# Kernel tuning notes

Hardware: AMD Instinct MI355X
Metric: run time of the kernel (lower is better)

## Reference

```python
import jax, jax.numpy as jnp
import numpy as np

N, F_IN, E = 20000, 256, 320000
H, C = 8, 128            # conv1 heads, per-head channels
OUT, DH = 1, 128         # output_dim, dense_hidden
G = 64                   # number of graphs
EPS = 1e-5


def setup_inputs() -> dict:
    key = jax.random.key(0)
    ks = jax.random.split(key, 20)
    s = 0.05
    return {
        'x': jax.random.normal(ks[0], (N, F_IN), jnp.float32),
        'edge_index': jax.random.randint(ks[1], (2, E), 0, N, jnp.int64),
        'batch': jnp.sort(jax.random.randint(ks[2], (N,), 0, G, jnp.int64)),
        # conv1 (GATv2, heads=8, concat)
        'w1_l': jax.random.normal(ks[3], (F_IN, H * C), jnp.float32) * s,
        'w1_r': jax.random.normal(ks[4], (F_IN, H * C), jnp.float32) * s,
        'att1': jax.random.normal(ks[5], (H, C), jnp.float32) * s,
        'b1': jnp.zeros((H * C,), jnp.float32),
        # norm1 (BatchNorm over H*C features)
        'g1': jnp.ones((H * C,), jnp.float32),
        'be1': jnp.zeros((H * C,), jnp.float32),
        # conv2 (GATv2, heads=1, concat=False)
        'w2_l': jax.random.normal(ks[6], (H * C, OUT), jnp.float32) * s,
        'w2_r': jax.random.normal(ks[7], (H * C, OUT), jnp.float32) * s,
        'att2': jax.random.normal(ks[8], (1, OUT), jnp.float32) * s,
        'b2': jnp.zeros((OUT,), jnp.float32),
        # norm2
        'g2': jnp.ones((OUT,), jnp.float32),
        'be2': jnp.zeros((OUT,), jnp.float32),
        # MLP head
        'lw1': jax.random.normal(ks[9], (OUT, DH), jnp.float32) * s,
        'lb1': jnp.zeros((DH,), jnp.float32),
        'lw2': jax.random.normal(ks[10], (DH, OUT), jnp.float32) * s,
        'lb2': jnp.zeros((OUT,), jnp.float32),
    }


def gatv2(x, src, dst, wl, wr, att, bias, heads, ch, concat):
    n = x.shape[0]
    xl = (x @ wl).reshape(n, heads, ch)
    xr = (x @ wr).reshape(n, heads, ch)
    # edge-wise GATv2 score: a^T LeakyReLU(x_l[j] + x_r[i]), slope 0.2
    e = jnp.einsum('ehc,hc->eh', jax.nn.leaky_relu(xl[src] + xr[dst], 0.2), att)
    # segment softmax over incoming edges per target node
    emax = jax.ops.segment_max(e, dst, num_segments=n)
    ee = jnp.exp(e - emax[dst])
    denom = jax.ops.segment_sum(ee, dst, num_segments=n)
    alpha = ee / (denom[dst] + 1e-16)
    out = jax.ops.segment_sum(alpha[..., None] * xl[src], dst, num_segments=n)  # [n,h,c]
    if concat:
        return out.reshape(n, heads * ch) + bias
    return out.mean(axis=1) + bias


def batchnorm(x, g, b):
    mu = x.mean(axis=0)
    var = ((x - mu) ** 2).mean(axis=0)
    return (x - mu) * jax.lax.rsqrt(var + EPS) * g + b


def reference(x, edge_index, batch, w1_l, w1_r, att1, b1, g1, be1,
              w2_l, w2_r, att2, b2, g2, be2, lw1, lb1, lw2, lb2):
    n = x.shape[0]
    loops = jnp.arange(n, dtype=edge_index.dtype)
    src = jnp.concatenate([edge_index[0], loops])  # add self-loops (PyG default)
    dst = jnp.concatenate([edge_index[1], loops])

    h = gatv2(x, src, dst, w1_l, w1_r, att1, b1, H, C, concat=True)
    h = jax.nn.leaky_relu(batchnorm(h, g1, be1), 0.01)
    # dropout: eval mode (identity)
    h = gatv2(h, src, dst, w2_l, w2_r, att2, b2, 1, OUT, concat=False)
    h = jax.nn.leaky_relu(batchnorm(h, g2, be2), 0.01)

    # global mean pool over graphs
    sums = jax.ops.segment_sum(h, batch, num_segments=G)
    cnt = jax.ops.segment_sum(jnp.ones((n, 1), h.dtype), batch, num_segments=G)
    pooled = sums / jnp.maximum(cnt, 1.0)

    out = jax.nn.leaky_relu(pooled @ lw1 + lb1, 0.01)
    return out @ lw2 + lb2
```

## Files before the change

kernel.cpp:

```cpp
#include <hip/hip_runtime.h>
#include <hip/hip_bf16.h>


__device__ __forceinline__ float lrelu(float x, float s) { return x > 0.f ? x : s * x; }

typedef _Float16 half8 __attribute__((ext_vector_type(8)));
typedef _Float16 half4v __attribute__((ext_vector_type(4)));
typedef _Float16 half2v __attribute__((ext_vector_type(2)));
typedef float f32x4 __attribute__((ext_vector_type(4)));

#define GLOBAL_AS __attribute__((address_space(1)))
#define LDS_AS __attribute__((address_space(3)))

__device__ __forceinline__ void async_copy16(const void* g, void* l) {
  __builtin_amdgcn_global_load_lds((const GLOBAL_AS unsigned int*)g,
                                   (LDS_AS unsigned int*)l, 16, 0, 0);
}

__global__ void zero_ints(int* __restrict__ p, int n) {
  const int t = blockIdx.x * blockDim.x + threadIdx.x;
  if (t < n) p[t] = 0;
}

__global__ void edge_hist(const int* __restrict__ ei, int E, int N,
                          int* __restrict__ counts) {
  const int t = blockIdx.x * blockDim.x + threadIdx.x;
  if (t >= E + N) return;
  const int dst = (t < E) ? ei[E + t] : (t - E);
  atomicAdd(&counts[dst], 1);
}

__global__ __launch_bounds__(1024) void scan_counts(const int* __restrict__ counts,
                                                    int* __restrict__ row_ptr,
                                                    int* __restrict__ cursor, int N) {
  __shared__ int sdata[1024];
  __shared__ int lcnt[20480];
  const int t = threadIdx.x;
  if (N <= 20480) {
    for (int j = t; j < N; j += 1024) lcnt[j] = counts[j];
    __syncthreads();
    const int chunk = (N + 1023) / 1024;
    const int s0 = min(N, t * chunk);
    const int s1 = min(N, s0 + chunk);
    int lsum = 0;
    for (int i = s0; i < s1; ++i) lsum += lcnt[i];
    sdata[t] = lsum;
    __syncthreads();
    for (int off = 1; off < 1024; off <<= 1) {
      int v = 0;
      if (t >= off) v = sdata[t - off];
      __syncthreads();
      sdata[t] += v;
      __syncthreads();
    }
    int run = sdata[t] - lsum;
    for (int i = s0; i < s1; ++i) { const int c = lcnt[i]; lcnt[i] = run; run += c; }
    if (s0 < N && s1 == N) row_ptr[N] = run;
    __syncthreads();
    for (int j = t; j < N; j += 1024) {
      const int v = lcnt[j];
      row_ptr[j] = v;
      cursor[j] = v;
    }
  } else {
    const int chunk = (N + 1023) / 1024;
    const int s0 = min(N, t * chunk);
    const int s1 = min(N, s0 + chunk);
    int lsum = 0;
    for (int i = s0; i < s1; ++i) lsum += counts[i];
    sdata[t] = lsum;
    __syncthreads();
    for (int off = 1; off < 1024; off <<= 1) {
      int v = 0;
      if (t >= off) v = sdata[t - off];
      __syncthreads();
      sdata[t] += v;
      __syncthreads();
    }
    int run = sdata[t] - lsum;
    for (int i = s0; i < s1; ++i) {
      row_ptr[i] = run;
      cursor[i] = run;
      run += counts[i];
    }
    if (s0 < N && s1 == N) row_ptr[N] = run;
  }
}

__global__ void edge_scatter(const int* __restrict__ ei, int E, int N,
                             int* __restrict__ cursor, int* __restrict__ col) {
  const int t = blockIdx.x * blockDim.x + threadIdx.x;
  if (t >= E + N) return;
  const int dst = (t < E) ? ei[E + t] : (t - E);
  const int src = (t < E) ? ei[t] : (t - E);
  const int pos = atomicAdd(&cursor[dst], 1);
  col[pos] = src;
}

__global__ void convert_x(const float* __restrict__ x, _Float16* __restrict__ A2, int M) {
  const int t = blockIdx.x * blockDim.x + threadIdx.x;
  if (t >= M * 64) return;
  const int m = t >> 6;
  const int k4 = (t & 63) * 4;
  const float4 v = *(const float4*)(x + (size_t)m * 256 + k4);
  const float sx = 16.f;
  *(half4v*)(A2 + (size_t)m * 256 + k4) =
      (half4v){(_Float16)(v.x * sx), (_Float16)(v.y * sx),
               (_Float16)(v.z * sx), (_Float16)(v.w * sx)};
}

__global__ __launch_bounds__(256) void convert_w(const float* __restrict__ wl,
                                                 const float* __restrict__ wr,
                                                 _Float16* __restrict__ B2,
                                                 int colOff, int W) {
  const int n = blockIdx.x;
  const int k = threadIdx.x;
  const float v = 16.f * ((n < W) ? wl[k * 1024 + colOff + n]
                                  : wr[k * 1024 + colOff + (n - W)]);
  B2[(size_t)n * 256 + k] = (_Float16)v;
}

__global__ __launch_bounds__(256) void gemm_mfma(const _Float16* __restrict__ A2,
                                                 const _Float16* __restrict__ B2,
                                                 _Float16* __restrict__ C,
                                                 int M, int Ntot) {
  __shared__ __align__(16) _Float16 LDSbuf[2 * 128 * 64];
  _Float16* As = LDSbuf;
  _Float16* Bs = LDSbuf + 128 * 64;
  const int tid = threadIdx.x;
  const int lane = tid & 63;
  const int wv = tid >> 6;
  const int wm = wv & 1, wn = wv >> 1;
  const int m_blk = blockIdx.y * 128;
  const int n_blk = blockIdx.x * 128;
  const int row16 = lane & 15, quad = lane >> 4;
  f32x4 acc[4][4] = {};

  for (int kt = 0; kt < 4; ++kt) {
    const int kg = kt * 64;
#pragma unroll
    for (int j = 0; j < 4; ++j) {
      const int ci = j * 256 + tid;
      const int row = ci >> 3;
      const int c = ci & 7;
      const int gc = c ^ (row & 7);
      _Float16* ldsA = &As[(j * 256 + wv * 64) * 8];
      _Float16* ldsB = &Bs[(j * 256 + wv * 64) * 8];
      const int growA = min(m_blk + row, M - 1);
      async_copy16(A2 + (size_t)growA * 256 + kg + gc * 8, ldsA);
      async_copy16(B2 + (size_t)(n_blk + row) * 256 + kg + gc * 8, ldsB);
    }
    __syncthreads();
#pragma unroll
    for (int ks = 0; ks < 2; ++ks) {
      half8 af[4], bf[4];
#pragma unroll
      for (int mi = 0; mi < 4; ++mi) {
        const int r = wm * 64 + mi * 16 + row16;
        const int cl = (ks * 4 + quad) ^ (r & 7);
        af[mi] = *(const half8*)&As[r * 64 + cl * 8];
      }
#pragma unroll
      for (int ni = 0; ni < 4; ++ni) {
        const int r = wn * 64 + ni * 16 + row16;
        const int cl = (ks * 4 + quad) ^ (r & 7);
        bf[ni] = *(const half8*)&Bs[r * 64 + cl * 8];
      }
#pragma unroll
      for (int mi = 0; mi < 4; ++mi)
#pragma unroll
        for (int ni = 0; ni < 4; ++ni)
          acc[mi][ni] = __builtin_amdgcn_mfma_f32_16x16x32_f16(af[mi], bf[ni], acc[mi][ni], 0, 0, 0);
    }
    __syncthreads();
  }
  const float inv = 1.f / 256.f;
  _Float16* tw = LDSbuf + wv * 4096;
#pragma unroll
  for (int mi = 0; mi < 4; ++mi)
#pragma unroll
    for (int reg = 0; reg < 4; ++reg) {
      const int r_in = mi * 16 + quad * 4 + reg;
#pragma unroll
      for (int ni = 0; ni < 4; ++ni)
        tw[r_in * 64 + ni * 16 + row16] = (_Float16)(acc[mi][ni][reg] * inv);
    }
#pragma unroll
  for (int p8 = 0; p8 < 8; ++p8) {
    const int row = p8 * 8 + (lane >> 3);
    const int grow = m_blk + wm * 64 + row;
    if (grow < M) {
      const half8 v = *(const half8*)&tw[row * 64 + (lane & 7) * 8];
      *(half8*)(C + (size_t)grow * Ntot + n_blk + wn * 64 + (lane & 7) * 8) = v;
    }
  }
}

template <int CPT>
__global__ __launch_bounds__(256, 6) void conv1_attn(const _Float16* __restrict__ xlrp,
                                                     const int* __restrict__ row_ptr,
                                                     const int* __restrict__ col,
                                                     const float* __restrict__ att,
                                                     const float* __restrict__ bias,
                                                     _Float16* __restrict__ h1,
                                                     int W, int N) {
  constexpr int PAIRS = CPT / 2;
  constexpr int NV8 = CPT / 8;
  constexpr int HG = 128 / CPT;
  union H8 { half8 v; half2v p[4]; };
  const int lane = threadIdx.x & 63;
  const int i = blockIdx.x * 4 + (threadIdx.x >> 6);
  if (i >= N) return;
  const int f = lane * CPT;
  half2v a2[PAIRS], xr2[PAIRS];
  float acc[CPT];
#pragma unroll
  for (int p = 0; p < PAIRS; ++p)
    a2[p] = (half2v){(_Float16)att[f + 2 * p], (_Float16)att[f + 2 * p + 1]};
  {
    const half8* xrp = (const half8*)(xlrp + (size_t)i * (2 * W) + W + f);
#pragma unroll
    for (int j = 0; j < NV8; ++j) {
      H8 u; u.v = xrp[j];
#pragma unroll
      for (int k = 0; k < 4; ++k) xr2[j * 4 + k] = u.p[k];
    }
  }
#pragma unroll
  for (int c = 0; c < CPT; ++c) acc[c] = 0.f;
  float m = -3.0e38f, l = 0.f;
  const int kb = row_ptr[i];
  const int ke = row_ptr[i + 1];
  for (int base = kb; base < ke; base += 64) {
    const int cnt = min(64, ke - base);
    const int myc = (lane < cnt) ? col[base + lane] : 0;
    H8 xc[NV8], xn[NV8];
    {
      const int s0 = __shfl(myc, 0);
      const half8* rp = (const half8*)(xlrp + (size_t)s0 * (2 * W) + f);
#pragma unroll
      for (int j = 0; j < NV8; ++j) xc[j].v = rp[j];
    }
    for (int q = 0; q < cnt; ++q) {
      if (q + 1 < cnt) {
        const int sn = __shfl(myc, q + 1);
        const half8* rp = (const half8*)(xlrp + (size_t)sn * (2 * W) + f);
#pragma unroll
        for (int j = 0; j < NV8; ++j) xn[j].v = rp[j];
      }
      float s = 0.f;
#pragma unroll
      for (int p = 0; p < PAIRS; ++p) {
        const half2v xp = xc[p >> 2].p[p & 3];
        const half2v t = xp + xr2[p];
        const half2v t5 = t * (half2v){(_Float16)0.2f, (_Float16)0.2f};
        const half2v lr = __builtin_elementwise_max(t, t5);
        s = __builtin_amdgcn_fdot2(a2[p], lr, s, false);
      }
#pragma unroll
      for (int off = HG / 2; off >= 1; off >>= 1) s += __shfl_xor(s, off);
      if (s <= m) {
        const float pw = __expf(s - m);
        l += pw;
#pragma unroll
        for (int p = 0; p < PAIRS; ++p) {
          const half2v xp = xc[p >> 2].p[p & 3];
          acc[2 * p] += pw * (float)xp[0];
          acc[2 * p + 1] += pw * (float)xp[1];
        }
      } else {
        const float sc = __expf(m - s);
        m = s;
        l = l * sc + 1.f;
#pragma unroll
        for (int p = 0; p < PAIRS; ++p) {
          const half2v xp = xc[p >> 2].p[p & 3];
          acc[2 * p] = acc[2 * p] * sc + (float)xp[0];
          acc[2 * p + 1] = acc[2 * p + 1] * sc + (float)xp[1];
        }
      }
#pragma unroll
      for (int j = 0; j < NV8; ++j) xc[j] = xn[j];
    }
  }
  const float inv = 1.f / (l + 1e-16f);
  _Float16* outp = h1 + (size_t)i * 1024 + f;
#pragma unroll
  for (int j = 0; j < NV8; ++j) {
    H8 u;
#pragma unroll
    for (int k = 0; k < 4; ++k) {
      const int c = j * 8 + 2 * k;
      u.p[k] = (half2v){(_Float16)(acc[c] * inv + bias[f + c]),
                        (_Float16)(acc[c + 1] * inv + bias[f + c + 1])};
    }
    ((half8*)outp)[j] = u.v;
  }
}

__global__ __launch_bounds__(256) void bn1_stats(const _Float16* __restrict__ h1,
                                                 float* __restrict__ bsum,
                                                 float* __restrict__ bsq, int N) {
  const int f = threadIdx.x * 4;
  const int chunk = (N + 255) / 256;
  const int r0 = blockIdx.y * chunk;
  const int r1 = min(N, r0 + chunk);
  float s0 = 0.f, s1 = 0.f, s2 = 0.f, s3 = 0.f;
  float q0 = 0.f, q1 = 0.f, q2 = 0.f, q3 = 0.f;
  for (int r = r0; r < r1; ++r) {
    const half4v v4 = *(const half4v*)(h1 + (size_t)r * 1024 + f);
    const float v0 = (float)v4[0], v1 = (float)v4[1], v2 = (float)v4[2], v3 = (float)v4[3];
    s0 += v0; q0 += v0 * v0;
    s1 += v1; q1 += v1 * v1;
    s2 += v2; q2 += v2 * v2;
    s3 += v3; q3 += v3 * v3;
  }
  atomicAdd(&bsum[f + 0], s0); atomicAdd(&bsq[f + 0], q0);
  atomicAdd(&bsum[f + 1], s1); atomicAdd(&bsq[f + 1], q1);
  atomicAdd(&bsum[f + 2], s2); atomicAdd(&bsq[f + 2], q2);
  atomicAdd(&bsum[f + 3], s3); atomicAdd(&bsq[f + 3], q3);
}

__global__ __launch_bounds__(256) void bn1_proj(const _Float16* __restrict__ h1,
                                                const float* __restrict__ bsum,
                                                const float* __restrict__ bsq,
                                                const float* __restrict__ g1,
                                                const float* __restrict__ be1,
                                                const float* __restrict__ w2l,
                                                const float* __restrict__ w2r,
                                                float* __restrict__ xl2,
                                                float* __restrict__ xr2, int N) {
  const int i = blockIdx.x;
  const int tid = threadIdx.x;
  const int f = tid * 4;
  const half4v hv = *(const half4v*)(h1 + (size_t)i * 1024 + f);
  const float4 h4 = make_float4((float)hv[0], (float)hv[1], (float)hv[2], (float)hv[3]);
  const float4 s4 = *(const float4*)(bsum + f);
  const float4 q4 = *(const float4*)(bsq + f);
  const float4 g4 = *(const float4*)(g1 + f);
  const float4 b4 = *(const float4*)(be1 + f);
  const float4 wl = *(const float4*)(w2l + f);
  const float4 wr = *(const float4*)(w2r + f);
  const float invN = 1.f / (float)N;
  float pl = 0.f, pr = 0.f;
  {
    float mu, var, rs, v;
    mu = s4.x * invN; var = q4.x * invN - mu * mu; rs = 1.f / sqrtf(var + 1e-5f);
    v = lrelu((h4.x - mu) * rs * g4.x + b4.x, 0.01f); pl += v * wl.x; pr += v * wr.x;
    mu = s4.y * invN; var = q4.y * invN - mu * mu; rs = 1.f / sqrtf(var + 1e-5f);
    v = lrelu((h4.y - mu) * rs * g4.y + b4.y, 0.01f); pl += v * wl.y; pr += v * wr.y;
    mu = s4.z * invN; var = q4.z * invN - mu * mu; rs = 1.f / sqrtf(var + 1e-5f);
    v = lrelu((h4.z - mu) * rs * g4.z + b4.z, 0.01f); pl += v * wl.z; pr += v * wr.z;
    mu = s4.w * invN; var = q4.w * invN - mu * mu; rs = 1.f / sqrtf(var + 1e-5f);
    v = lrelu((h4.w - mu) * rs * g4.w + b4.w, 0.01f); pl += v * wl.w; pr += v * wr.w;
  }
#pragma unroll
  for (int off = 32; off; off >>= 1) {
    pl += __shfl_down(pl, off);
    pr += __shfl_down(pr, off);
  }
  __shared__ float sp[8];
  if ((tid & 63) == 0) {
    sp[tid >> 6] = pl;
    sp[4 + (tid >> 6)] = pr;
  }
  __syncthreads();
  if (tid == 0) {
    xl2[i] = sp[0] + sp[1] + sp[2] + sp[3];
    xr2[i] = sp[4] + sp[5] + sp[6] + sp[7];
  }
}

__global__ __launch_bounds__(256) void conv2_attn(const float* __restrict__ xl2,
                                                  const float* __restrict__ xr2,
                                                  const int* __restrict__ row_ptr,
                                                  const int* __restrict__ col,
                                                  const float* __restrict__ att2,
                                                  const float* __restrict__ b2,
                                                  float* __restrict__ out2,
                                                  float* __restrict__ bn2acc, int N) {
  const int i = blockIdx.x * blockDim.x + threadIdx.x;
  float val = 0.f;
  if (i < N) {
    const float a = att2[0];
    const float xr = xr2[i];
    float m = -3.0e38f, l = 0.f, acc = 0.f;
    const int kb = row_ptr[i];
    const int ke = row_ptr[i + 1];
    for (int k = kb; k < ke; ++k) {
      const float xv = xl2[col[k]];
      const float s = a * lrelu(xv + xr, 0.2f);
      const float mn = fmaxf(m, s);
      const float sc = __expf(m - mn);
      const float p = __expf(s - mn);
      l = l * sc + p;
      acc = acc * sc + p * xv;
      m = mn;
    }
    val = acc / (l + 1e-16f) + b2[0];
    out2[i] = val;
  }
  float s = (i < N) ? val : 0.f;
  float q = s * s;
#pragma unroll
  for (int off = 32; off; off >>= 1) {
    s += __shfl_down(s, off);
    q += __shfl_down(q, off);
  }
  __shared__ float red[8];
  if ((threadIdx.x & 63) == 0) {
    red[threadIdx.x >> 6] = s;
    red[4 + (threadIdx.x >> 6)] = q;
  }
  __syncthreads();
  if (threadIdx.x == 0) {
    atomicAdd(&bn2acc[0], red[0] + red[1] + red[2] + red[3]);
    atomicAdd(&bn2acc[1], red[4] + red[5] + red[6] + red[7]);
  }
}

__global__ __launch_bounds__(256) void bn2_pool(const float* __restrict__ out2,
                                                const float* __restrict__ bn2acc,
                                                const float* __restrict__ g2,
                                                const float* __restrict__ be2,
                                                const int* __restrict__ batch,
                                                float* __restrict__ pool_sum,
                                                float* __restrict__ pool_cnt, int N) {
  __shared__ float ls[64];
  __shared__ float lc[64];
  const int tid = threadIdx.x;
  if (tid < 64) { ls[tid] = 0.f; lc[tid] = 0.f; }
  __syncthreads();
  const int i = blockIdx.x * blockDim.x + tid;
  if (i < N) {
    const float invN = 1.f / (float)N;
    const float mu = bn2acc[0] * invN;
    const float var = bn2acc[1] * invN - mu * mu;
    const float rs = 1.f / sqrtf(var + 1e-5f);
    const float v = lrelu((out2[i] - mu) * rs * g2[0] + be2[0], 0.01f);
    const int g = batch[i];
    atomicAdd(&ls[g], v);
    atomicAdd(&lc[g], 1.f);
  }
  __syncthreads();
  if (tid < 64 && lc[tid] != 0.f) {
    atomicAdd(&pool_sum[tid], ls[tid]);
    atomicAdd(&pool_cnt[tid], lc[tid]);
  }
}

__global__ void head_mlp(const float* __restrict__ pool_sum, const float* __restrict__ pool_cnt,
                         const float* __restrict__ lw1, const float* __restrict__ lb1,
                         const float* __restrict__ lw2, const float* __restrict__ lb2,
                         float* __restrict__ out) {
  const int g = threadIdx.x;
  if (g >= 64) return;
  const float p = pool_sum[g] / fmaxf(pool_cnt[g], 1.f);
  float acc = 0.f;
  for (int d = 0; d < 128; ++d) {
    float t = p * lw1[d] + lb1[d];
    t = lrelu(t, 0.01f);
    acc += t * lw2[d];
  }
  out[g] = acc + lb2[0];
}

extern "C" void kernel_launch(void* const* d_in, const int* in_sizes, int n_in,
                              void* d_out, int out_size, void* d_ws, size_t ws_size,
                              hipStream_t stream) {
  const float* x = (const float*)d_in[0];
  const int* ei = (const int*)d_in[1];
  const int* batch = (const int*)d_in[2];
  const float* w1_l = (const float*)d_in[3];
  const float* w1_r = (const float*)d_in[4];
  const float* att1 = (const float*)d_in[5];
  const float* b1 = (const float*)d_in[6];
  const float* g1 = (const float*)d_in[7];
  const float* be1 = (const float*)d_in[8];
  const float* w2_l = (const float*)d_in[9];
  const float* w2_r = (const float*)d_in[10];
  const float* att2 = (const float*)d_in[11];
  const float* b2 = (const float*)d_in[12];
  const float* g2 = (const float*)d_in[13];
  const float* be2 = (const float*)d_in[14];
  const float* lw1 = (const float*)d_in[15];
  const float* lb1 = (const float*)d_in[16];
  const float* lw2 = (const float*)d_in[17];
  const float* lb2 = (const float*)d_in[18];

  const int N = in_sizes[2];
  const int E = in_sizes[1] / 2;
  const int ET = E + N;

  const size_t AL = 255;
  auto al = [&](size_t b) { return (b + AL) & ~AL; };
  const size_t zbytes = (size_t)N * 4 + 4096 + 4096 + 16 + 256 + 256;
  const size_t fixedNoXlr = al((size_t)N * 2048)
                          + 3 * al((size_t)N * 4)
                          + al((size_t)(N + 1) * 4)
                          + al((size_t)ET * 4)
                          + al((size_t)N * 4)
                          + al(zbytes);
  const size_t a2b = al((size_t)N * 256 * 2);
  int P = 1;
  while (P < 8) {
    const size_t xlrb = al((size_t)N * (4096 / P));
    const size_t b2b = al((size_t)(2 * (1024 / P)) * 256 * 2);
    const size_t extra = (P == 1) ? 0 : (a2b + b2b);
    if (fixedNoXlr + xlrb + extra <= ws_size) break;
    P <<= 1;
  }
  const int W = 1024 / P;

  char* ws = (char*)d_ws;
  size_t off = 0;
  auto alloc = [&](size_t b) { size_t p = off; off += al(b); return p; };
  _Float16* h1 = (_Float16*)(ws + alloc((size_t)N * 2048));
  _Float16* xlrp = (_Float16*)(ws + alloc((size_t)N * (4096 / P)));
  float* xl2 = (float*)(ws + alloc((size_t)N * 4));
  float* xr2 = (float*)(ws + alloc((size_t)N * 4));
  float* out2 = (float*)(ws + alloc((size_t)N * 4));
  int* row_ptr = (int*)(ws + alloc((size_t)(N + 1) * 4));
  int* colb = (int*)(ws + alloc((size_t)ET * 4));
  int* cursor = (int*)(ws + alloc((size_t)N * 4));
  char* zbase = ws + alloc(zbytes);
  int* counts = (int*)zbase;
  float* bn1_sum = (float*)(zbase + (size_t)N * 4);
  float* bn1_sq = (float*)(zbase + (size_t)N * 4 + 4096);
  float* bn2acc = (float*)(zbase + (size_t)N * 4 + 8192);
  float* pool_sum = (float*)(zbase + (size_t)N * 4 + 8192 + 16);
  float* pool_cnt = (float*)(zbase + (size_t)N * 4 + 8192 + 16 + 256);

  _Float16 *A2, *B2;
  if (P == 1) {
    A2 = (_Float16*)h1;
    B2 = (_Float16*)((char*)h1 + a2b);
  } else {
    A2 = (_Float16*)(ws + alloc((size_t)N * 256 * 2));
    B2 = (_Float16*)(ws + alloc((size_t)(2 * W) * 256 * 2));
  }

  const int zn = (int)(zbytes / 4);
  zero_ints<<<(zn + 255) / 256, 256, 0, stream>>>((int*)zbase, zn);

  edge_hist<<<(ET + 255) / 256, 256, 0, stream>>>(ei, E, N, counts);
  scan_counts<<<1, 1024, 0, stream>>>(counts, row_ptr, cursor, N);
  edge_scatter<<<(ET + 255) / 256, 256, 0, stream>>>(ei, E, N, cursor, colb);

  convert_x<<<(N * 64 + 255) / 256, 256, 0, stream>>>(x, A2, N);
  for (int p = 0; p < P; ++p) {
    convert_w<<<2 * W, 256, 0, stream>>>(w1_l, w1_r, B2, p * W, W);
    gemm_mfma<<<dim3(2 * W / 128, (N + 127) / 128), 256, 0, stream>>>(A2, B2, xlrp, N, 2 * W);
    if (W >= 1024)
      conv1_attn<16><<<(N + 3) / 4, 256, 0, stream>>>(xlrp, row_ptr, colb,
                                                      att1 + p * W, b1 + p * W,
                                                      h1 + p * W, W, N);
    else
      conv1_attn<8><<<(N + 3) / 4, 256, 0, stream>>>(xlrp, row_ptr, colb,
                                                     att1 + p * W, b1 + p * W,
                                                     h1 + p * W, W, N);
  }

  bn1_stats<<<dim3(1, 256), 256, 0, stream>>>(h1, bn1_sum, bn1_sq, N);
  bn1_proj<<<N, 256, 0, stream>>>(h1, bn1_sum, bn1_sq, g1, be1, w2_l, w2_r, xl2, xr2, N);
  conv2_attn<<<(N + 255) / 256, 256, 0, stream>>>(xl2, xr2, row_ptr, colb, att2, b2,
                                                  out2, bn2acc, N);
  bn2_pool<<<(N + 255) / 256, 256, 0, stream>>>(out2, bn2acc, g2, be2, batch, pool_sum, pool_cnt, N);
  head_mlp<<<1, 64, 0, stream>>>(pool_sum, pool_cnt, lw1, lb1, lw2, lb2, (float*)d_out);
}
```

Baseline: 393.3 us.

## Split conv1 attention per node across two waves with software-prefetched gathers

Adds a dedicated conv1 attention kernel for the full-width case. Each node is handled by two wavefronts, each covering 512 features at 8 per lane, instead of one wavefront at 16 per lane. The kernel prefetches the next neighbor's source row while it computes the current one and runs an online softmax. The goal is more parallelism and hidden gather latency. The cost is duplicated index loads and score reductions per node, plus a hardcoded layout where the row stride is 2048.

```diff
diff --git a/kernel.cpp b/kernel.cpp
--- a/kernel.cpp
+++ b/kernel.cpp
@@ -194,6 +194,94 @@
       *(half8*)(C + (size_t)grow * Ntot + n_blk + wn * 64 + (lane & 7) * 8) = v;
     }
   }
+}
+
+__global__ __launch_bounds__(256, 8) void conv1_attn_hw(const _Float16* __restrict__ xlrp,
+                                                        const int* __restrict__ row_ptr,
+                                                        const int* __restrict__ col,
+                                                        const float* __restrict__ att,
+                                                        const float* __restrict__ bias,
+                                                        _Float16* __restrict__ h1, int N) {
+  union H8 { half8 v; half2v p[4]; };
+  const int wv = threadIdx.x >> 6;
+  const int lane = threadIdx.x & 63;
+  const int i = blockIdx.x * 2 + (wv >> 1);
+  if (i >= N) return;
+  const int f = (wv & 1) * 512 + lane * 8;
+  half2v a2[4], xr2[4];
+  float acc[8];
+#pragma unroll
+  for (int p = 0; p < 4; ++p)
+    a2[p] = (half2v){(_Float16)att[f + 2 * p], (_Float16)att[f + 2 * p + 1]};
+  {
+    H8 u;
+    u.v = *(const half8*)(xlrp + (size_t)i * 2048 + 1024 + f);
+#pragma unroll
+    for (int k = 0; k < 4; ++k) xr2[k] = u.p[k];
+  }
+#pragma unroll
+  for (int c = 0; c < 8; ++c) acc[c] = 0.f;
+  float m = -3.0e38f, l = 0.f;
+  const int kb = row_ptr[i];
+  const int ke = row_ptr[i + 1];
+  for (int base = kb; base < ke; base += 64) {
+    const int cnt = min(64, ke - base);
+    const int myc = (lane < cnt) ? col[base + lane] : 0;
+    H8 xc, xn;
+    {
+      const int s0 = __shfl(myc, 0);
+      xc.v = *(const half8*)(xlrp + (size_t)s0 * 2048 + f);
+    }
+    for (int q = 0; q < cnt; ++q) {
+      if (q + 1 < cnt) {
+        const int sn = __shfl(myc, q + 1);
+        xn.v = *(const half8*)(xlrp + (size_t)sn * 2048 + f);
+      }
+      float s = 0.f;
+#pragma unroll
+      for (int p = 0; p < 4; ++p) {
+        const half2v xp = xc.p[p];
+        const half2v t = xp + xr2[p];
+        const half2v t5 = t * (half2v){(_Float16)0.2f, (_Float16)0.2f};
+        const half2v lr = __builtin_elementwise_max(t, t5);
+        s = __builtin_amdgcn_fdot2(a2[p], lr, s, false);
+      }
+      s += __shfl_xor(s, 8);
+      s += __shfl_xor(s, 4);
+      s += __shfl_xor(s, 2);
+      s += __shfl_xor(s, 1);
+      if (s <= m) {
+        const float pw = __expf(s - m);
+        l += pw;
+#pragma unroll
+        for (int p = 0; p < 4; ++p) {
+          const half2v xp = xc.p[p];
+          acc[2 * p] += pw * (float)xp[0];
+          acc[2 * p + 1] += pw * (float)xp[1];
+        }
+      } else {
+        const float sc = __expf(m - s);
+        m = s;
+        l = l * sc + 1.f;
+#pragma unroll
+        for (int p = 0; p < 4; ++p) {
+          const half2v xp = xc.p[p];
+          acc[2 * p] = acc[2 * p] * sc + (float)xp[0];
+          acc[2 * p + 1] = acc[2 * p + 1] * sc + (float)xp[1];
+        }
+      }
+      xc = xn;
+    }
+  }
+  const float inv = 1.f / (l + 1e-16f);
+  H8 u;
+#pragma unroll
+  for (int k = 0; k < 4; ++k) {
+    const int c = 2 * k;
+    u.p[k] = (half2v){(_Float16)(acc[c] * inv + bias[f + c]),
+                      (_Float16)(acc[c + 1] * inv + bias[f + c + 1])};
+  }
+  *(half8*)(h1 + (size_t)i * 1024 + f) = u.v;
 }
 
 template <int CPT>
@@ -552,9 +640,8 @@
     convert_w<<<2 * W, 256, 0, stream>>>(w1_l, w1_r, B2, p * W, W);
     gemm_mfma<<<dim3(2 * W / 128, (N + 127) / 128), 256, 0, stream>>>(A2, B2, xlrp, N, 2 * W);
     if (W >= 1024)
-      conv1_attn<16><<<(N + 3) / 4, 256, 0, stream>>>(xlrp, row_ptr, colb,
-                                                      att1 + p * W, b1 + p * W,
-                                                      h1 + p * W, W, N);
+      conv1_attn_hw<<<(N + 1) / 2, 256, 0, stream>>>(xlrp, row_ptr, colb,
+                                                     att1, b1, h1, N);
     else
       conv1_attn<8><<<(N + 3) / 4, 256, 0, stream>>>(xlrp, row_ptr, colb,
                                                      att1 + p * W, b1 + p * W,
```

New measurement: 388.0 us. Within noise of the previous version (-1.3%).
